# Optimization experiments

Measured on AMD Instinct MI355X. Metric: run time of the kernel, lower is better.

Reference implementation:

```python
import jax, jax.numpy as jnp
import numpy as np

INPUT_DIM = 512
HEAD_NUM = 8
ATT_SIZE = 64
EPS = 1e-5


def layer_norm(x, g, b):
    mu = jnp.mean(x, axis=-1, keepdims=True)
    var = jnp.mean(jnp.square(x - mu), axis=-1, keepdims=True)
    return (x - mu) * jax.lax.rsqrt(var + EPS) * g + b


def setup_inputs() -> dict:
    key = jax.random.key(0)
    ks = jax.random.split(key, 10)
    D, H, A = INPUT_DIM, HEAD_NUM, ATT_SIZE
    HA = H * A
    s = lambda fan_in: 1.0 / np.sqrt(fan_in)
    x = jax.random.normal(ks[0], (32, 6, 256, D), dtype=jnp.float32)
    # Linear weights stored as [in, out] so y = x @ W + b (matches torch x @ W.T)
    Wq = jax.random.uniform(ks[1], (D, HA), jnp.float32, -s(D), s(D))
    bq = jnp.zeros((HA,), jnp.float32)
    Wk = jax.random.uniform(ks[2], (D, HA), jnp.float32, -s(D), s(D))
    bk = jnp.zeros((HA,), jnp.float32)
    Wv = jax.random.uniform(ks[3], (D, HA), jnp.float32, -s(D), s(D))
    bv = jnp.zeros((HA,), jnp.float32)
    Wo = jax.random.uniform(ks[4], (HA, D), jnp.float32, -s(HA), s(HA))
    bo = jnp.zeros((D,), jnp.float32)
    g1 = jnp.ones((D,), jnp.float32)
    b1 = jnp.zeros((D,), jnp.float32)
    Wd = jax.random.uniform(ks[5], (2 * D, D), jnp.float32, -s(2 * D), s(2 * D))
    bd = jnp.zeros((D,), jnp.float32)
    g2 = jnp.ones((D,), jnp.float32)
    b2 = jnp.zeros((D,), jnp.float32)
    return dict(x=x, Wq=Wq, bq=bq, Wk=Wk, bk=bk, Wv=Wv, bv=bv,
                Wo=Wo, bo=bo, g1=g1, b1=b1, Wd=Wd, bd=bd, g2=g2, b2=b2)


def reference(x, Wq, bq, Wk, bk, Wv, bv, Wo, bo, g1, b1, Wd, bd, g2, b2):
    B, M, P, D = x.shape
    H, A = HEAD_NUM, ATT_SIZE
    # QKV projections -> [B, M, H, P, A]
    q = (x @ Wq + bq).reshape(B, M, P, H, A).transpose(0, 1, 3, 2, 4)
    k = (x @ Wk + bk).reshape(B, M, P, H, A).transpose(0, 1, 3, 2, 4)
    v = (x @ Wv + bv).reshape(B, M, P, H, A).transpose(0, 1, 3, 2, 4)
    scores = jnp.einsum('bmhqa,bmhka->bmhqk', q, k) / jnp.sqrt(jnp.float32(A))
    attn = jax.nn.softmax(scores, axis=-1)
    z = jnp.einsum('bmhqk,bmhka->bmhqa', attn, v)
    z = z.transpose(0, 1, 3, 2, 4).reshape(B, M, P, H * A)
    z = jax.nn.relu(x + layer_norm(z @ Wo + bo, g1, b1))
    # patch merge (1/2 downsample)
    if P % 2:  # static shape check, fine under jit
        z = jnp.pad(z, ((0, 0), (0, 0), (0, 1), (0, 0)))
    merged = jnp.concatenate([z[:, :, 0::2, :], z[:, :, 1::2, :]], axis=-1)
    out = jax.nn.relu(layer_norm(merged @ Wd + bd, g2, b2))
    return out
```

## Files before the change

kernel.cpp:

```cpp
#include <hip/hip_runtime.h>
#include <hip/hip_bf16.h>
#include <stdint.h>


typedef __hip_bfloat16 bf16;
typedef __attribute__((ext_vector_type(8))) __bf16 bf16v8;
typedef __attribute__((ext_vector_type(4))) float f32x4;
typedef __attribute__((ext_vector_type(8))) short s16x8;
typedef __attribute__((ext_vector_type(4))) short s16x4;

static __device__ __forceinline__ void gl_lds16(const void* src, void* dst) {
  __builtin_amdgcn_global_load_lds((const __attribute__((address_space(1))) void*)src,
                                   (__attribute__((address_space(3))) void*)dst,
                                   16, 0, 0);
}

static __device__ __forceinline__ unsigned short f2bfu(float f) {
  return __builtin_bit_cast(unsigned short, __float2bfloat16(f));
}
static __device__ __forceinline__ float bfu2f(unsigned short u) {
  return __builtin_bit_cast(float, (unsigned int)u << 16);
}

__global__ __launch_bounds__(256) void conv_x_kernel(const float4* __restrict__ x,
                                                     s16x4* __restrict__ xb, int n4) {
  int stride = gridDim.x * 256;
  for (int i = blockIdx.x * 256 + threadIdx.x; i < n4; i += stride) {
    float4 v = x[i];
    s16x4 o;
    o[0] = (short)f2bfu(v.x); o[1] = (short)f2bfu(v.y);
    o[2] = (short)f2bfu(v.z); o[3] = (short)f2bfu(v.w);
    xb[i] = o;
  }
}

__global__ __launch_bounds__(256) void conv_w_kernel(
    const float* __restrict__ Wq, const float* __restrict__ Wk, const float* __restrict__ Wv,
    const float* __restrict__ Wo, const float* __restrict__ Wd,
    const float* __restrict__ bq, const float* __restrict__ bk, const float* __restrict__ bv,
    bf16* __restrict__ wqkv_t, bf16* __restrict__ wo_t, bf16* __restrict__ wd_t,
    float* __restrict__ bqkv) {
  int o = blockIdx.x * 256 + threadIdx.x;
  if (o < 786432) {
    int j = o >> 9, kk = o & 511;
    const float* W = (j < 512) ? Wq : (j < 1024) ? Wk : Wv;
    wqkv_t[o] = __float2bfloat16(W[kk * 512 + (j & 511)]);
  } else if (o < 1048576) {
    int o2 = o - 786432; int j = o2 >> 9, kk = o2 & 511;
    wo_t[o2] = __float2bfloat16(Wo[kk * 512 + j]);
  } else if (o < 1572864) {
    int o3 = o - 1048576; int j = o3 >> 10, kk = o3 & 1023;
    wd_t[o3] = __float2bfloat16(Wd[kk * 512 + j]);
  } else if (o < 1574400) {
    int o4 = o - 1572864;
    const float* b = (o4 < 512) ? bq : (o4 < 1024) ? bk : bv;
    bqkv[o4] = b[o4 & 511];
  }
}

template<int EPI, int AMODE>
__global__ __launch_bounds__(512, 2) void gemm256(
    const bf16* __restrict__ A, const bf16* __restrict__ Bt,
    const float* __restrict__ bias, int K,
    bf16* __restrict__ oq, bf16* __restrict__ ok, bf16* __restrict__ ovt,
    bf16* __restrict__ obf, float* __restrict__ of) {
  __shared__ __align__(16) char smem[131072];
  const int tid = threadIdx.x;
  const int wave = tid >> 6, lane = tid & 63;
  const int wr = wave >> 2, wc = wave & 3;
  const int lane15 = lane & 15, g = lane >> 4;
  const int tileM = blockIdx.x * 256, tileN = blockIdx.y * 256;

  const int rT = tid >> 3;
  const int cT = (tid & 7) ^ (rT & 7);

  const int nkt = K >> 6;
  const int iters = nkt >> 1;

  auto stage = [&](int tau, int q) {
    char* dst = smem + ((tau & 1) << 16) + ((q >> 1) << 15) + ((q & 1) << 14) + tid * 16;
    int kpos = tau * 64 + cT * 8;
    if (q < 2) {
      int rowA = tileM + ((q & 1) << 7) + rT;
      if (AMODE == 0) {
        const bf16* s0 = A + (size_t)rowA * K + kpos;
        gl_lds16(s0, dst);
        gl_lds16(s0 + (size_t)64 * K, dst + 8192);
      } else {
#pragma unroll
        for (int j = 0; j < 2; ++j) {
          int mr = rowA + j * 64;
          int bm = mr >> 7, pp = mr & 127;
          const bf16* s = A + (size_t)(bm * 256 + pp * 2 + (kpos >> 9)) * 512 + (kpos & 511);
          gl_lds16(s, dst + j * 8192);
        }
      }
    } else {
      int rowB = tileN + ((q & 1) << 7) + rT;
      const bf16* s0 = Bt + (size_t)rowB * K + kpos;
      gl_lds16(s0, dst);
      gl_lds16(s0 + (size_t)64 * K, dst + 8192);
    }
  };

  f32x4 acc[8][4] = {};
  bf16v8 areg[4][2], breg[2][2];

  stage(0, 0); stage(0, 1); stage(0, 2); stage(0, 3);
  stage(1, 0); stage(1, 1);
  asm volatile("s_waitcnt vmcnt(4)" ::: "memory");
  __builtin_amdgcn_s_barrier();

  for (int it = 0; it < iters; ++it) {
    const bool last = (it == iters - 1);
#pragma unroll
    for (int p = 0; p < 8; ++p) {
      const int buf = p >> 2;
      const int mh = (p >> 1) & 1, nh = p & 1;
      char* Ab = smem + (buf << 16);
      char* Bb = Ab + 32768;
      if (nh == 0) {
#pragma unroll
        for (int f = 0; f < 4; ++f) {
          int row = wr * 128 + (mh * 4 + f) * 16 + lane15;
#pragma unroll
          for (int ks = 0; ks < 2; ++ks)
            areg[f][ks] = *(const bf16v8*)(Ab + row * 128 + (((ks * 4 + g) ^ (row & 7)) << 4));
        }
      }
#pragma unroll
      for (int n = 0; n < 2; ++n) {
        int row = wc * 64 + (nh * 2 + n) * 16 + lane15;
#pragma unroll
        for (int ks = 0; ks < 2; ++ks)
          breg[n][ks] = *(const bf16v8*)(Bb + row * 128 + (((ks * 4 + g) ^ (row & 7)) << 4));
      }
      if (p == 0)      { stage(2 * it + 1, 2); stage(2 * it + 1, 3); }
      else if (p == 3) { if (!last) { stage(2 * it + 2, 0); stage(2 * it + 2, 1); } }
      else if (p == 4) { if (!last) { stage(2 * it + 2, 2); stage(2 * it + 2, 3); } }
      else if (p == 7) { if (!last) { stage(2 * it + 3, 0); stage(2 * it + 3, 1); } }
      __builtin_amdgcn_s_barrier();
      asm volatile("s_waitcnt lgkmcnt(0)" ::: "memory");
      __builtin_amdgcn_s_setprio(1);
#pragma unroll
      for (int ks = 0; ks < 2; ++ks)
#pragma unroll
        for (int f = 0; f < 4; ++f)
#pragma unroll
          for (int n = 0; n < 2; ++n)
            acc[mh * 4 + f][nh * 2 + n] = __builtin_amdgcn_mfma_f32_16x16x32_bf16(
                areg[f][ks], breg[n][ks], acc[mh * 4 + f][nh * 2 + n], 0, 0, 0);
      __builtin_amdgcn_s_setprio(0);
      if (p == 3) {
        if (last) { asm volatile("s_waitcnt vmcnt(0)" ::: "memory"); }
        else      { asm volatile("s_waitcnt vmcnt(4)" ::: "memory"); }
      } else if (p == 7) {
        if (!last) { asm volatile("s_waitcnt vmcnt(4)" ::: "memory"); }
      }
      __builtin_amdgcn_s_barrier();
    }
  }

  if (EPI == 0 && tileN >= 1024) {
    const int hh = ((tileN - 1024) >> 6) + wc;
    const int bm = tileM >> 8;
    char* slab = smem + wave * 16384;
#pragma unroll
    for (int fm = 0; fm < 8; ++fm) {
#pragma unroll
      for (int fn = 0; fn < 4; ++fn) {
        int col = tileN + wc * 64 + fn * 16 + lane15;
        float bb = bias[col];
        int a = fn * 16 + lane15;
#pragma unroll
        for (int i = 0; i < 4; ++i) {
          int pl = fm * 16 + g * 4 + i;
          *(bf16*)(slab + a * 256 + ((pl * 2) ^ ((a & 7) << 4))) =
              __float2bfloat16(acc[fm][fn][i] + bb);
        }
      }
    }
    bf16* vdst = ovt + ((size_t)(bm * 8 + hh) << 14) + wr * 128;
#pragma unroll
    for (int r = 0; r < 16; ++r) {
      int a = r * 4 + (lane >> 4);
      int ps = lane & 15;
      s16x8 vv = *(const s16x8*)(slab + a * 256 + ((ps * 16) ^ ((a & 7) << 4)));
      *(s16x8*)(vdst + a * 256 + ps * 8) = vv;
    }
  } else {
#pragma unroll
    for (int fm = 0; fm < 8; ++fm) {
#pragma unroll
      for (int fn = 0; fn < 4; ++fn) {
        int col = tileN + wc * 64 + fn * 16 + lane15;
        float bb = bias[col];
#pragma unroll
        for (int i = 0; i < 4; ++i) {
          int row = tileM + wr * 128 + fm * 16 + g * 4 + i;
          float val = acc[fm][fn][i] + bb;
          if (EPI == 0) {
            int bm = row >> 8, p = row & 255;
            int hh = col >> 6, a = col & 63;
            if (col < 512) {
              oq[((size_t)(bm * 8 + hh) << 14) + (p << 6) + a] = __float2bfloat16(val);
            } else {
              int j = col - 512; hh = j >> 6; a = j & 63;
              ok[((size_t)(bm * 8 + hh) << 14) + (p << 6) + a] = __float2bfloat16(val);
            }
          } else if (EPI == 1) {
            obf[(size_t)row * 512 + col] = __float2bfloat16(val);
          } else {
            of[(size_t)row * 512 + col] = val;
          }
        }
      }
    }
  }
}

__global__ __launch_bounds__(256) void attn_kernel(const bf16* __restrict__ q,
                                                   const bf16* __restrict__ k,
                                                   const bf16* __restrict__ vt,
                                                   bf16* __restrict__ z) {
  __shared__ __align__(16) char smem[81920];
  const int tid = threadIdx.x, wave = tid >> 6, lane = tid & 63;
  const int lane15 = lane & 15, g = lane >> 4;
  const int qc = blockIdx.x, hh = blockIdx.y, bm = blockIdx.z;
  const int bh = bm * 8 + hh;
  const bf16* kbase = k + ((size_t)bh << 14);
  const bf16* vbase = vt + ((size_t)bh << 14);
  const bf16* qbase = q + ((size_t)bh << 14) + (qc * 64 + wave * 16) * 64;

#pragma unroll
  for (int i = 0; i < 8; ++i) {
    int s = i * 256 + tid;
    int kr = s >> 3, ksp = s & 7;
    gl_lds16(kbase + kr * 64 + (ksp ^ (kr & 7)) * 8, smem + s * 16);
    int ar = s >> 5, asp = s & 31;
    gl_lds16(vbase + ar * 256 + (asp ^ (ar & 7)) * 8, smem + 32768 + s * 16);
  }
  bf16v8 qf[2];
#pragma unroll
  for (int kk = 0; kk < 2; ++kk)
    qf[kk] = *(const bf16v8*)(qbase + lane15 * 64 + kk * 32 + g * 8);
  __syncthreads();

  f32x4 sacc[16] = {};
#pragma unroll
  for (int tl = 0; tl < 16; ++tl) {
    int key = tl * 16 + lane15;
    int rb = key * 128, swk = (key & 7) << 4;
#pragma unroll
    for (int kk = 0; kk < 2; ++kk) {
      bf16v8 kf = *(const bf16v8*)(smem + rb + (((kk * 4 + g) * 16) ^ swk));
      sacc[tl] = __builtin_amdgcn_mfma_f32_16x16x32_bf16(qf[kk], kf, sacc[tl], 0, 0, 0);
    }
  }

  float mx[4], sm[4], rcp[4];
#pragma unroll
  for (int i = 0; i < 4; ++i) mx[i] = sacc[0][i];
#pragma unroll
  for (int tl = 1; tl < 16; ++tl)
#pragma unroll
    for (int i = 0; i < 4; ++i) mx[i] = fmaxf(mx[i], sacc[tl][i]);
#pragma unroll
  for (int i = 0; i < 4; ++i) {
    mx[i] = fmaxf(mx[i], __shfl_xor(mx[i], 1));
    mx[i] = fmaxf(mx[i], __shfl_xor(mx[i], 2));
    mx[i] = fmaxf(mx[i], __shfl_xor(mx[i], 4));
    mx[i] = fmaxf(mx[i], __shfl_xor(mx[i], 8));
    sm[i] = 0.f;
  }
#pragma unroll
  for (int tl = 0; tl < 16; ++tl)
#pragma unroll
    for (int i = 0; i < 4; ++i) {
      float e = __expf((sacc[tl][i] - mx[i]) * 0.125f);
      sacc[tl][i] = e; sm[i] += e;
    }
#pragma unroll
  for (int i = 0; i < 4; ++i) {
    sm[i] += __shfl_xor(sm[i], 1);
    sm[i] += __shfl_xor(sm[i], 2);
    sm[i] += __shfl_xor(sm[i], 4);
    sm[i] += __shfl_xor(sm[i], 8);
    rcp[i] = 1.0f / sm[i];
  }

  char* pbase = smem + 65536 + wave * 4096;
  f32x4 oacc[4] = {};
#pragma unroll
  for (int h2 = 0; h2 < 2; ++h2) {
#pragma unroll
    for (int t8 = 0; t8 < 8; ++t8) {
      int tl = h2 * 8 + t8;
#pragma unroll
      for (int i = 0; i < 4; ++i) {
        int r = g * 4 + i;
        int c2 = t8 * 16 + lane15;
        *(bf16*)(pbase + r * 256 + ((c2 * 2) ^ ((r & 7) << 4))) =
            __float2bfloat16(sacc[tl][i] * rcp[i]);
      }
    }
    asm volatile("" ::: "memory");
#pragma unroll
    for (int k2 = 0; k2 < 4; ++k2) {
      int ks = h2 * 4 + k2;
      bf16v8 pf = *(const bf16v8*)(pbase + lane15 * 256 +
                                   ((k2 * 64 + g * 16) ^ ((lane15 & 7) << 4)));
#pragma unroll
      for (int at = 0; at < 4; ++at) {
        int a = at * 16 + lane15;
        bf16v8 vf = *(const bf16v8*)(smem + 32768 + a * 512 +
                                     ((ks * 64 + g * 16) ^ ((a & 7) << 4)));
        oacc[at] = __builtin_amdgcn_mfma_f32_16x16x32_bf16(pf, vf, oacc[at], 0, 0, 0);
      }
    }
    asm volatile("" ::: "memory");
  }

  int trow = bm * 256 + qc * 64 + wave * 16;
#pragma unroll
  for (int at = 0; at < 4; ++at)
#pragma unroll
    for (int i = 0; i < 4; ++i)
      z[(size_t)(trow + g * 4 + i) * 512 + hh * 64 + at * 16 + lane15] =
          __float2bfloat16(oacc[at][i]);
}

static __device__ __forceinline__ float wredsum(float v) {
  v += __shfl_xor(v, 1);  v += __shfl_xor(v, 2);  v += __shfl_xor(v, 4);
  v += __shfl_xor(v, 8);  v += __shfl_xor(v, 16); v += __shfl_xor(v, 32);
  return v;
}

__global__ __launch_bounds__(256) void ln_res_kernel(const bf16* __restrict__ y1,
                                                     const float* __restrict__ x,
                                                     const float* __restrict__ g1,
                                                     const float* __restrict__ b1,
                                                     bf16* __restrict__ z2) {
  const int wave = threadIdx.x >> 6, lane = threadIdx.x & 63;
  const int row = blockIdx.x * 4 + wave;
  const size_t base = (size_t)row * 512 + lane * 8;
  s16x8 yv = *(const s16x8*)(y1 + base);
  float f[8];
#pragma unroll
  for (int j = 0; j < 8; ++j) f[j] = bfu2f((unsigned short)yv[j]);
  float s = 0.f, s2 = 0.f;
#pragma unroll
  for (int j = 0; j < 8; ++j) { s += f[j]; s2 += f[j] * f[j]; }
  s = wredsum(s); s2 = wredsum(s2);
  float mu = s * (1.f / 512.f);
  float var = s2 * (1.f / 512.f) - mu * mu;
  float rs = rsqrtf(var + 1e-5f);
  float4 x0 = *(const float4*)(x + base);
  float4 x1 = *(const float4*)(x + base + 4);
  float xa[8] = {x0.x, x0.y, x0.z, x0.w, x1.x, x1.y, x1.z, x1.w};
  float ga[8], ba[8];
#pragma unroll
  for (int j = 0; j < 8; ++j) { ga[j] = g1[lane * 8 + j]; ba[j] = b1[lane * 8 + j]; }
  s16x8 ov;
#pragma unroll
  for (int j = 0; j < 8; ++j) {
    float v = xa[j] + (f[j] - mu) * rs * ga[j] + ba[j];
    ov[j] = (short)f2bfu(fmaxf(v, 0.f));
  }
  *(s16x8*)(z2 + base) = ov;
}

__global__ __launch_bounds__(256) void ln_out_kernel(const float* __restrict__ y2,
                                                     const float* __restrict__ g2,
                                                     const float* __restrict__ b2,
                                                     float* __restrict__ out) {
  const int wave = threadIdx.x >> 6, lane = threadIdx.x & 63;
  const int row = blockIdx.x * 4 + wave;
  const size_t base = (size_t)row * 512 + lane * 8;
  float4 v0 = *(const float4*)(y2 + base);
  float4 v1 = *(const float4*)(y2 + base + 4);
  float f[8] = {v0.x, v0.y, v0.z, v0.w, v1.x, v1.y, v1.z, v1.w};
  float s = 0.f, s2 = 0.f;
#pragma unroll
  for (int j = 0; j < 8; ++j) { s += f[j]; s2 += f[j] * f[j]; }
  s = wredsum(s); s2 = wredsum(s2);
  float mu = s * (1.f / 512.f);
  float var = s2 * (1.f / 512.f) - mu * mu;
  float rs = rsqrtf(var + 1e-5f);
  float o[8];
#pragma unroll
  for (int j = 0; j < 8; ++j)
    o[j] = fmaxf((f[j] - mu) * rs * g2[lane * 8 + j] + b2[lane * 8 + j], 0.f);
  float4 w0 = {o[0], o[1], o[2], o[3]};
  float4 w1 = {o[4], o[5], o[6], o[7]};
  *(float4*)(out + base) = w0;
  *(float4*)(out + base + 4) = w1;
}

extern "C" void kernel_launch(void* const* d_in, const int* in_sizes, int n_in,
                              void* d_out, int out_size, void* d_ws, size_t ws_size,
                              hipStream_t stream) {
  const float* x  = (const float*)d_in[0];
  const float* Wq = (const float*)d_in[1];
  const float* bq = (const float*)d_in[2];
  const float* Wk = (const float*)d_in[3];
  const float* bk = (const float*)d_in[4];
  const float* Wv = (const float*)d_in[5];
  const float* bv = (const float*)d_in[6];
  const float* Wo = (const float*)d_in[7];
  const float* bo = (const float*)d_in[8];
  const float* g1 = (const float*)d_in[9];
  const float* b1 = (const float*)d_in[10];
  const float* Wd = (const float*)d_in[11];
  const float* bd = (const float*)d_in[12];
  const float* g2 = (const float*)d_in[13];
  const float* b2 = (const float*)d_in[14];

  char* ws = (char*)d_ws;
  const size_t SEG = 50331648;
  bf16*  xb   = (bf16*)(ws);
  bf16*  qb   = (bf16*)(ws + SEG);
  bf16*  kb   = (bf16*)(ws + 2 * SEG);
  bf16*  vtb  = (bf16*)(ws + 3 * SEG);
  bf16*  wqkv = (bf16*)(ws + 4 * SEG);
  bf16*  wot  = (bf16*)(ws + 4 * SEG + 1572864);
  bf16*  wdt  = (bf16*)(ws + 4 * SEG + 2097152);
  float* bqkv = (float*)(ws + 4 * SEG + 3145728);
  bf16*  zb   = xb;
  bf16*  y1   = qb;
  bf16*  z2   = kb;
  float* y2   = (float*)vtb;

  conv_x_kernel<<<4096, 256, 0, stream>>>((const float4*)x, (s16x4*)xb, 25165824 / 4);
  conv_w_kernel<<<6150, 256, 0, stream>>>(Wq, Wk, Wv, Wo, Wd, bq, bk, bv,
                                          wqkv, wot, wdt, bqkv);
  gemm256<0, 0><<<dim3(192, 6), 512, 0, stream>>>(xb, wqkv, bqkv, 512,
                                                  qb, kb, vtb, nullptr, nullptr);
  attn_kernel<<<dim3(4, 8, 192), 256, 0, stream>>>(qb, kb, vtb, zb);
  gemm256<1, 0><<<dim3(192, 2), 512, 0, stream>>>(zb, wot, bo, 512,
                                                  nullptr, nullptr, nullptr, y1, nullptr);
  ln_res_kernel<<<12288, 256, 0, stream>>>(y1, x, g1, b1, z2);
  gemm256<2, 1><<<dim3(96, 2), 512, 0, stream>>>(z2, wdt, bd, 1024,
                                                 nullptr, nullptr, nullptr, nullptr, y2);
  ln_out_kernel<<<6144, 256, 0, stream>>>(y2, g2, b2, (float*)d_out);
}
```

Before: 348.8 us.

## Cut GEMM main-loop barriers, stage epilogue through LDS, store final GEMM in bf16

The GEMM main loop now places barriers only at the phases where LDS buffers are reused, instead of two barriers per phase. The Q/K and plain-output epilogues are staged through a swizzled LDS slab so global stores become coalesced 16-byte writes instead of scattered 2-byte stores. The last GEMM now writes bf16 instead of fp32, halving intermediate traffic into the final layernorm. Risks are LDS races if the reduced barrier placement is wrong, and the extra rounding of the pre-layernorm activations to bf16.

```diff
diff --git a/kernel.cpp b/kernel.cpp
--- a/kernel.cpp
+++ b/kernel.cpp
@@ -63,7 +63,7 @@
     const bf16* __restrict__ A, const bf16* __restrict__ Bt,
     const float* __restrict__ bias, int K,
     bf16* __restrict__ oq, bf16* __restrict__ ok, bf16* __restrict__ ovt,
-    bf16* __restrict__ obf, float* __restrict__ of) {
+    bf16* __restrict__ obf) {
   __shared__ __align__(16) char smem[131072];
   const int tid = threadIdx.x;
   const int wave = tid >> 6, lane = tid & 63;
@@ -74,8 +74,7 @@
   const int rT = tid >> 3;
   const int cT = (tid & 7) ^ (rT & 7);
 
-  const int nkt = K >> 6;
-  const int iters = nkt >> 1;
+  const int iters = K >> 7;
 
   auto stage = [&](int tau, int q) {
     char* dst = smem + ((tau & 1) << 16) + ((q >> 1) << 15) + ((q & 1) << 14) + tid * 16;
@@ -139,8 +138,6 @@
       else if (p == 3) { if (!last) { stage(2 * it + 2, 0); stage(2 * it + 2, 1); } }
       else if (p == 4) { if (!last) { stage(2 * it + 2, 2); stage(2 * it + 2, 3); } }
       else if (p == 7) { if (!last) { stage(2 * it + 3, 0); stage(2 * it + 3, 1); } }
-      __builtin_amdgcn_s_barrier();
-      asm volatile("s_waitcnt lgkmcnt(0)" ::: "memory");
       __builtin_amdgcn_s_setprio(1);
 #pragma unroll
       for (int ks = 0; ks < 2; ++ks)
@@ -151,13 +148,18 @@
             acc[mh * 4 + f][nh * 2 + n] = __builtin_amdgcn_mfma_f32_16x16x32_bf16(
                 areg[f][ks], breg[n][ks], acc[mh * 4 + f][nh * 2 + n], 0, 0, 0);
       __builtin_amdgcn_s_setprio(0);
-      if (p == 3) {
-        if (last) { asm volatile("s_waitcnt vmcnt(0)" ::: "memory"); }
-        else      { asm volatile("s_waitcnt vmcnt(4)" ::: "memory"); }
+      if (p == 2 || p == 6) {
+        asm volatile("s_waitcnt lgkmcnt(0)" ::: "memory");
+        __builtin_amdgcn_s_barrier();
+      } else if (p == 3) {
+        if (last) { asm volatile("s_waitcnt vmcnt(0) lgkmcnt(0)" ::: "memory"); }
+        else      { asm volatile("s_waitcnt vmcnt(4) lgkmcnt(0)" ::: "memory"); }
+        __builtin_amdgcn_s_barrier();
       } else if (p == 7) {
-        if (!last) { asm volatile("s_waitcnt vmcnt(4)" ::: "memory"); }
-      }
-      __builtin_amdgcn_s_barrier();
+        if (last) { asm volatile("s_waitcnt lgkmcnt(0)" ::: "memory"); }
+        else      { asm volatile("s_waitcnt vmcnt(4) lgkmcnt(0)" ::: "memory"); }
+        __builtin_amdgcn_s_barrier();
+      }
     }
   }
 
@@ -180,6 +182,7 @@
         }
       }
     }
+    asm volatile("" ::: "memory");
     bf16* vdst = ovt + ((size_t)(bm * 8 + hh) << 14) + wr * 128;
 #pragma unroll
     for (int r = 0; r < 16; ++r) {
@@ -189,32 +192,40 @@
       *(s16x8*)(vdst + a * 256 + ps * 8) = vv;
     }
   } else {
+    char* slab = smem + wave * 16384;
 #pragma unroll
     for (int fm = 0; fm < 8; ++fm) {
 #pragma unroll
       for (int fn = 0; fn < 4; ++fn) {
         int col = tileN + wc * 64 + fn * 16 + lane15;
         float bb = bias[col];
+        int lb = (fn * 16 + lane15) * 2;
 #pragma unroll
         for (int i = 0; i < 4; ++i) {
-          int row = tileM + wr * 128 + fm * 16 + g * 4 + i;
-          float val = acc[fm][fn][i] + bb;
-          if (EPI == 0) {
-            int bm = row >> 8, p = row & 255;
-            int hh = col >> 6, a = col & 63;
-            if (col < 512) {
-              oq[((size_t)(bm * 8 + hh) << 14) + (p << 6) + a] = __float2bfloat16(val);
-            } else {
-              int j = col - 512; hh = j >> 6; a = j & 63;
-              ok[((size_t)(bm * 8 + hh) << 14) + (p << 6) + a] = __float2bfloat16(val);
-            }
-          } else if (EPI == 1) {
-            obf[(size_t)row * 512 + col] = __float2bfloat16(val);
-          } else {
-            of[(size_t)row * 512 + col] = val;
-          }
+          int pl = fm * 16 + g * 4 + i;
+          *(bf16*)(slab + pl * 128 + (lb ^ ((((pl >> 2) & 3)) << 5))) =
+              __float2bfloat16(acc[fm][fn][i] + bb);
         }
       }
+    }
+    asm volatile("" ::: "memory");
+    bf16* dst; int ldc2;
+    if (EPI == 0) {
+      int cb = tileN + wc * 64;
+      int hh = (cb >> 6) & 7;
+      bf16* base = (cb < 512) ? oq : ok;
+      dst = base + (((size_t)((tileM >> 8) * 8 + hh)) << 14) + wr * 128 * 64;
+      ldc2 = 64;
+    } else {
+      dst = obf + (size_t)(tileM + wr * 128) * 512 + tileN + wc * 64;
+      ldc2 = 512;
+    }
+#pragma unroll
+    for (int r = 0; r < 16; ++r) {
+      int s = r * 64 + lane;
+      int pl = s >> 3, sl = s & 7;
+      s16x8 vv = *(const s16x8*)(slab + pl * 128 + ((sl * 16) ^ ((((pl >> 2) & 3)) << 5)));
+      *(s16x8*)(dst + (size_t)pl * ldc2 + sl * 8) = vv;
     }
   }
 }
@@ -370,16 +381,17 @@
   *(s16x8*)(z2 + base) = ov;
 }
 
-__global__ __launch_bounds__(256) void ln_out_kernel(const float* __restrict__ y2,
+__global__ __launch_bounds__(256) void ln_out_kernel(const bf16* __restrict__ y2,
                                                      const float* __restrict__ g2,
                                                      const float* __restrict__ b2,
                                                      float* __restrict__ out) {
   const int wave = threadIdx.x >> 6, lane = threadIdx.x & 63;
   const int row = blockIdx.x * 4 + wave;
   const size_t base = (size_t)row * 512 + lane * 8;
-  float4 v0 = *(const float4*)(y2 + base);
-  float4 v1 = *(const float4*)(y2 + base + 4);
-  float f[8] = {v0.x, v0.y, v0.z, v0.w, v1.x, v1.y, v1.z, v1.w};
+  s16x8 yv = *(const s16x8*)(y2 + base);
+  float f[8];
+#pragma unroll
+  for (int j = 0; j < 8; ++j) f[j] = bfu2f((unsigned short)yv[j]);
   float s = 0.f, s2 = 0.f;
 #pragma unroll
   for (int j = 0; j < 8; ++j) { s += f[j]; s2 += f[j] * f[j]; }
@@ -429,18 +441,18 @@
   bf16*  zb   = xb;
   bf16*  y1   = qb;
   bf16*  z2   = kb;
-  float* y2   = (float*)vtb;
+  bf16*  y2   = vtb;
 
   conv_x_kernel<<<4096, 256, 0, stream>>>((const float4*)x, (s16x4*)xb, 25165824 / 4);
   conv_w_kernel<<<6150, 256, 0, stream>>>(Wq, Wk, Wv, Wo, Wd, bq, bk, bv,
                                           wqkv, wot, wdt, bqkv);
   gemm256<0, 0><<<dim3(192, 6), 512, 0, stream>>>(xb, wqkv, bqkv, 512,
-                                                  qb, kb, vtb, nullptr, nullptr);
+                                                  qb, kb, vtb, nullptr);
   attn_kernel<<<dim3(4, 8, 192), 256, 0, stream>>>(qb, kb, vtb, zb);
   gemm256<1, 0><<<dim3(192, 2), 512, 0, stream>>>(zb, wot, bo, 512,
-                                                  nullptr, nullptr, nullptr, y1, nullptr);
+                                                  nullptr, nullptr, nullptr, y1);
   ln_res_kernel<<<12288, 256, 0, stream>>>(y1, x, g1, b1, z2);
-  gemm256<2, 1><<<dim3(96, 2), 512, 0, stream>>>(z2, wdt, bd, 1024,
-                                                 nullptr, nullptr, nullptr, nullptr, y2);
+  gemm256<1, 1><<<dim3(96, 2), 512, 0, stream>>>(z2, wdt, bd, 1024,
+                                                 nullptr, nullptr, nullptr, y2);
   ln_out_kernel<<<6144, 256, 0, stream>>>(y2, g2, b2, (float*)d_out);
 }
```

Result: faster. 337.6 us (-3.2%).
